# Kernel tuning notes

Hardware: AMD Instinct MI355X
Metric: run time of the kernel (lower is better)

The kernel has to match this reference:

```python
import jax, jax.numpy as jnp
import numpy as np

N = 4_000_000

def setup_inputs() -> dict:
    key = jax.random.key(0)
    k1, k2 = jax.random.split(key)
    scaling_raw = jax.random.normal(k1, (N, 3), dtype=jnp.float32) * 0.5 - 3.0  # log-scales
    rotation = jax.random.normal(k2, (N, 4), dtype=jnp.float32)
    return {"scaling_raw": scaling_raw, "rotation": rotation}

def build_rotation(r):
    # r: (N,4) unnormalized quaternion (w,x,y,z)
    q = r / jnp.linalg.norm(r, axis=-1, keepdims=True)
    w, x, y, z = q[:, 0], q[:, 1], q[:, 2], q[:, 3]
    R = jnp.stack([
        1 - 2 * (y * y + z * z), 2 * (x * y - w * z),     2 * (x * z + w * y),
        2 * (x * y + w * z),     1 - 2 * (x * x + z * z), 2 * (y * z - w * x),
        2 * (x * z - w * y),     2 * (y * z + w * x),     1 - 2 * (x * x + y * y),
    ], axis=-1).reshape(-1, 3, 3)
    return R

def reference(scaling_raw, rotation):
    scaling_modifier = 1.0
    s = scaling_modifier * jnp.exp(scaling_raw)  # (N,3)
    R = build_rotation(rotation)                  # (N,3,3)
    L = R * s[:, None, :]                         # R @ diag(s)
    cov = jnp.einsum('nij,nkj->nik', L, L)        # L @ L^T, (N,3,3)
    # strip_symmetric: upper triangle [00,01,02,11,12,22]
    symm = jnp.stack([cov[:, 0, 0], cov[:, 0, 1], cov[:, 0, 2],
                      cov[:, 1, 1], cov[:, 1, 2], cov[:, 2, 2]], axis=-1)
    return symm
```

## Files before the change

kernel.cpp:

```cpp
#include <hip/hip_runtime.h>


__global__ __launch_bounds__(256) void gauss_cov_kernel(
    const float* __restrict__ sr,
    const float4* __restrict__ rot,
    float* __restrict__ out,
    int n)
{
    int stride = gridDim.x * blockDim.x;
    for (int i = blockIdx.x * blockDim.x + threadIdx.x; i < n; i += stride) {
        float4 q = rot[i];
        float inv = rsqrtf(q.x * q.x + q.y * q.y + q.z * q.z + q.w * q.w);
        float w = q.x * inv, x = q.y * inv, y = q.z * inv, z = q.w * inv;

        size_t si = (size_t)i * 3;
        float s0 = expf(sr[si + 0]);
        float s1 = expf(sr[si + 1]);
        float s2 = expf(sr[si + 2]);

        float xx = x * x, yy = y * y, zz = z * z;
        float xy = x * y, xz = x * z, yz = y * z;
        float wx = w * x, wy = w * y, wz = w * z;

        float R00 = 1.f - 2.f * (yy + zz), R01 = 2.f * (xy - wz), R02 = 2.f * (xz + wy);
        float R10 = 2.f * (xy + wz), R11 = 1.f - 2.f * (xx + zz), R12 = 2.f * (yz - wx);
        float R20 = 2.f * (xz - wy), R21 = 2.f * (yz + wx), R22 = 1.f - 2.f * (xx + yy);

        float L00 = R00 * s0, L01 = R01 * s1, L02 = R02 * s2;
        float L10 = R10 * s0, L11 = R11 * s1, L12 = R12 * s2;
        float L20 = R20 * s0, L21 = R21 * s1, L22 = R22 * s2;

        float c00 = L00 * L00 + L01 * L01 + L02 * L02;
        float c01 = L00 * L10 + L01 * L11 + L02 * L12;
        float c02 = L00 * L20 + L01 * L21 + L02 * L22;
        float c11 = L10 * L10 + L11 * L11 + L12 * L12;
        float c12 = L10 * L20 + L11 * L21 + L12 * L22;
        float c22 = L20 * L20 + L21 * L21 + L22 * L22;

        float2* o = (float2*)(out + (size_t)i * 6);
        o[0] = make_float2(c00, c01);
        o[1] = make_float2(c02, c11);
        o[2] = make_float2(c12, c22);
    }
}

extern "C" void kernel_launch(void* const* d_in, const int* in_sizes, int n_in,
                              void* d_out, int out_size, void* d_ws, size_t ws_size,
                              hipStream_t stream) {
    const float*  sr  = (const float*)d_in[0];
    const float4* rot = (const float4*)d_in[1];
    float* out = (float*)d_out;
    int n = in_sizes[0] / 3;

    const int block = 256;
    int grid = (n + block - 1) / block;
    if (grid > 2048) grid = 2048;
    gauss_cov_kernel<<<grid, block, 0, stream>>>(sr, rot, out, n);
}
```

Before: 183.4 us.

## Process four Gaussians per thread with float4 loads and stores

Each thread now handles four consecutive Gaussians, loading scales as three float4, quaternions as four float4, and writing outputs as six float4. It also replaces expf with the fast __expf and drops the grid-stride loop cap in favour of one thread per four elements. The goal is fewer, wider memory transactions and more bytes in flight per thread. Costs are higher register use, a strided per-thread access pattern, and a scalar tail path; __expf is slightly less accurate.

```diff
diff --git a/kernel.cpp b/kernel.cpp
--- a/kernel.cpp
+++ b/kernel.cpp
@@ -1,46 +1,65 @@
 #include <hip/hip_runtime.h>
 
 
-__global__ __launch_bounds__(256) void gauss_cov_kernel(
+__device__ __forceinline__ void cov6(float w, float x, float y, float z,
+                                     float s0, float s1, float s2,
+                                     float* __restrict__ c) {
+    float inv = rsqrtf(w * w + x * x + y * y + z * z);
+    w *= inv; x *= inv; y *= inv; z *= inv;
+    float xx = x * x, yy = y * y, zz = z * z;
+    float xy = x * y, xz = x * z, yz = y * z;
+    float wx = w * x, wy = w * y, wz = w * z;
+    float L00 = (1.f - 2.f * (yy + zz)) * s0, L01 = 2.f * (xy - wz) * s1, L02 = 2.f * (xz + wy) * s2;
+    float L10 = 2.f * (xy + wz) * s0, L11 = (1.f - 2.f * (xx + zz)) * s1, L12 = 2.f * (yz - wx) * s2;
+    float L20 = 2.f * (xz - wy) * s0, L21 = 2.f * (yz + wx) * s1, L22 = (1.f - 2.f * (xx + yy)) * s2;
+    c[0] = L00 * L00 + L01 * L01 + L02 * L02;
+    c[1] = L00 * L10 + L01 * L11 + L02 * L12;
+    c[2] = L00 * L20 + L01 * L21 + L02 * L22;
+    c[3] = L10 * L10 + L11 * L11 + L12 * L12;
+    c[4] = L10 * L20 + L11 * L21 + L12 * L22;
+    c[5] = L20 * L20 + L21 * L21 + L22 * L22;
+}
+
+__global__ __launch_bounds__(256) void gauss_cov4_kernel(
+    const float4* __restrict__ sr4,
+    const float4* __restrict__ rot,
+    float4* __restrict__ out4,
     const float* __restrict__ sr,
-    const float4* __restrict__ rot,
     float* __restrict__ out,
     int n)
 {
-    int stride = gridDim.x * blockDim.x;
-    for (int i = blockIdx.x * blockDim.x + threadIdx.x; i < n; i += stride) {
-        float4 q = rot[i];
-        float inv = rsqrtf(q.x * q.x + q.y * q.y + q.z * q.z + q.w * q.w);
-        float w = q.x * inv, x = q.y * inv, y = q.z * inv, z = q.w * inv;
+    int t = blockIdx.x * 256 + threadIdx.x;
+    long long g = (long long)t * 4;
+    if (g + 3 < n) {
+        float4 a = sr4[3 * (size_t)t];
+        float4 b = sr4[3 * (size_t)t + 1];
+        float4 d = sr4[3 * (size_t)t + 2];
+        float4 q0 = rot[g], q1 = rot[g + 1], q2 = rot[g + 2], q3 = rot[g + 3];
 
-        size_t si = (size_t)i * 3;
-        float s0 = expf(sr[si + 0]);
-        float s1 = expf(sr[si + 1]);
-        float s2 = expf(sr[si + 2]);
+        float e0  = __expf(a.x), e1  = __expf(a.y), e2  = __expf(a.z);
+        float e3  = __expf(a.w), e4  = __expf(b.x), e5  = __expf(b.y);
+        float e6  = __expf(b.z), e7  = __expf(b.w), e8  = __expf(d.x);
+        float e9  = __expf(d.y), e10 = __expf(d.z), e11 = __expf(d.w);
 
-        float xx = x * x, yy = y * y, zz = z * z;
-        float xy = x * y, xz = x * z, yz = y * z;
-        float wx = w * x, wy = w * y, wz = w * z;
+        float c[24];
+        cov6(q0.x, q0.y, q0.z, q0.w, e0, e1, e2, c + 0);
+        cov6(q1.x, q1.y, q1.z, q1.w, e3, e4, e5, c + 6);
+        cov6(q2.x, q2.y, q2.z, q2.w, e6, e7, e8, c + 12);
+        cov6(q3.x, q3.y, q3.z, q3.w, e9, e10, e11, c + 18);
 
-        float R00 = 1.f - 2.f * (yy + zz), R01 = 2.f * (xy - wz), R02 = 2.f * (xz + wy);
-        float R10 = 2.f * (xy + wz), R11 = 1.f - 2.f * (xx + zz), R12 = 2.f * (yz - wx);
-        float R20 = 2.f * (xz - wy), R21 = 2.f * (yz + wx), R22 = 1.f - 2.f * (xx + yy);
-
-        float L00 = R00 * s0, L01 = R01 * s1, L02 = R02 * s2;
-        float L10 = R10 * s0, L11 = R11 * s1, L12 = R12 * s2;
-        float L20 = R20 * s0, L21 = R21 * s1, L22 = R22 * s2;
-
-        float c00 = L00 * L00 + L01 * L01 + L02 * L02;
-        float c01 = L00 * L10 + L01 * L11 + L02 * L12;
-        float c02 = L00 * L20 + L01 * L21 + L02 * L22;
-        float c11 = L10 * L10 + L11 * L11 + L12 * L12;
-        float c12 = L10 * L20 + L11 * L21 + L12 * L22;
-        float c22 = L20 * L20 + L21 * L21 + L22 * L22;
-
-        float2* o = (float2*)(out + (size_t)i * 6);
-        o[0] = make_float2(c00, c01);
-        o[1] = make_float2(c02, c11);
-        o[2] = make_float2(c12, c22);
+        float4* o = out4 + 6 * (size_t)t;
+        #pragma unroll
+        for (int j = 0; j < 6; ++j)
+            o[j] = make_float4(c[4 * j], c[4 * j + 1], c[4 * j + 2], c[4 * j + 3]);
+    } else if (g < n) {
+        for (long long i = g; i < n; ++i) {
+            float4 q = rot[i];
+            float e0 = __expf(sr[3 * i]), e1 = __expf(sr[3 * i + 1]), e2 = __expf(sr[3 * i + 2]);
+            float c[6];
+            cov6(q.x, q.y, q.z, q.w, e0, e1, e2, c);
+            #pragma unroll
+            for (int j = 0; j < 6; ++j) out[6 * i + j] = c[j];
+        }
     }
 }
 
@@ -52,8 +71,8 @@
     float* out = (float*)d_out;
     int n = in_sizes[0] / 3;
 
-    const int block = 256;
-    int grid = (n + block - 1) / block;
-    if (grid > 2048) grid = 2048;
-    gauss_cov_kernel<<<grid, block, 0, stream>>>(sr, rot, out, n);
+    int nthreads = (n + 3) / 4;
+    int grid = (nthreads + 255) / 256;
+    gauss_cov4_kernel<<<grid, 256, 0, stream>>>(
+        (const float4*)sr, rot, (float4*)out, sr, out, n);
 }
```

Result: slower. 193.2 us (+5.3%).
